# Kernel tuning notes

Measured on AMD Instinct MI355X. Metric: run time of the kernel, lower is better.

The kernel has to match this reference:

```python
import jax, jax.numpy as jnp
import numpy as np
from jax import lax

B, H, W = 2, 384, 384
NF = 64
SECTIONS = [2, 3, 4, 5, 6, 7, 8]  # radial core widths -> kernel sizes 3,5,7,9,11,13,15


def _radial_matrix(w):
    """Static [K,K,w] matrix mapping w radial core channels -> full KxK kernel,
    K = 2*w-1, replicating the torch nested-loop radial interpolation + flipcat."""
    mid = w - 1
    M = np.zeros((w, w, w), dtype=np.float32)
    for i in range(w):
        for j in range(w):
            d = np.sqrt(float((i - mid) ** 2 + (j - mid) ** 2))
            if d > mid:
                continue
            low, high = np.floor(d), np.ceil(d)
            if low == high:
                M[i, j, int(low)] = 1.0
            else:
                M[i, j, int(low)] = high - d
                M[i, j, int(low) + 1] = d - low
    # flipcat along both spatial dims: index order [0..w-1, w-2..0]
    q = mid - np.abs(np.arange(2 * w - 1) - mid)
    return M[q][:, q]  # [K, K, w]


def _conv(x, w, b):
    y = lax.conv_general_dilated(x, w, (1, 1), 'SAME',
                                 dimension_numbers=('NCHW', 'OIHW', 'NCHW'))
    return y + b[None, :, None, None]


def _resblock(x, wa, ba, wb, bb):
    return x + _conv(jax.nn.relu(_conv(x, wa, ba)), wb, bb)


def setup_inputs() -> dict:
    key = jax.random.key(0)
    ks = jax.random.split(key, 12)

    def wgt(k, shape):
        fan_in = shape[1] * shape[2] * shape[3]
        return jax.random.normal(k, shape, jnp.float32) / np.sqrt(fan_in)

    inp = {
        'data_with_est': jax.random.normal(ks[0], (B, 2, H, W), jnp.float32),
        'data': jax.random.normal(ks[1], (B, 1, H, W), jnp.float32),
        'w_first': wgt(ks[2], (NF, 2, 3, 3)), 'b_first': jnp.zeros((NF,), jnp.float32),
        'w1a': wgt(ks[3], (NF, NF, 3, 3)), 'b1a': jnp.zeros((NF,), jnp.float32),
        'w1b': wgt(ks[4], (NF, NF, 3, 3)), 'b1b': jnp.zeros((NF,), jnp.float32),
        'w2a': wgt(ks[5], (NF, NF, 3, 3)), 'b2a': jnp.zeros((NF,), jnp.float32),
        'w2b': wgt(ks[6], (NF, NF, 3, 3)), 'b2b': jnp.zeros((NF,), jnp.float32),
        'w3a': wgt(ks[7], (NF, NF, 3, 3)), 'b3a': jnp.zeros((NF,), jnp.float32),
        'w3b': wgt(ks[8], (NF, NF, 3, 3)), 'b3b': jnp.zeros((NF,), jnp.float32),
        'w_out': wgt(ks[9], (35, NF, 3, 3)), 'b_out': jnp.zeros((35,), jnp.float32),
    }
    return inp


def reference(data_with_est, data, w_first, b_first, w1a, b1a, w1b, b1b,
              w2a, b2a, w2b, b2b, w3a, b3a, w3b, b3b, w_out, b_out):
    # KPN backbone
    x = _conv(data_with_est, w_first, b_first)
    x = _resblock(x, w1a, b1a, w1b, b1b)
    x = _resblock(x, w2a, b2a, w2b, b2b)
    x = _resblock(x, w3a, b3a, w3b, b3b)
    core = _conv(x, w_out, b_out)  # [B, 35, H, W]

    frames = data[:, 0]  # [B, H, W]  (N=1, color=1)
    pred_img = jnp.zeros((B, H, W), core.dtype)
    off = 0
    for wsec in SECTIONS:
        K = 2 * wsec - 1
        r = K // 2
        M = jnp.asarray(_radial_matrix(wsec))  # [K, K, wsec]
        c = jnp.abs(lax.slice_in_dim(core, off, off + wsec, axis=1))  # [B, wsec, H, W]
        off += wsec
        # position-varying KxK kernel per pixel, softmax over the K*K taps
        kern = jnp.einsum('ijc,bchw->bijhw', M, c).reshape(B, K * K, H, W)
        kern = jax.nn.softmax(kern, axis=1)
        pad = jnp.pad(frames, ((0, 0), (r, r), (r, r)))
        # shifted neighborhood stack in torch loop order (i over rows, j over cols)
        patches = jnp.stack([pad[:, i:i + H, j:j + W]
                             for i in range(K) for j in range(K)], axis=1)
        pred_img = pred_img + jnp.sum(kern * patches, axis=1)
    return pred_img[:, None]  # [B, 1, H, W]
```

## Files before the change

### kernel.cpp

```cpp
#include <hip/hip_runtime.h>

#define HH 384
#define WW 384
#define BB 2

typedef unsigned short ushort_t;
typedef short  s16x8 __attribute__((ext_vector_type(8)));
typedef float  f32x4 __attribute__((ext_vector_type(4)));
typedef int    i32x4 __attribute__((ext_vector_type(4)));
typedef int    i32x2 __attribute__((ext_vector_type(2)));

union V16 { i32x4 i4; s16x8 v; ushort_t h[8]; };
union V8  { i32x2 i2; ushort_t h[4]; };

__device__ __forceinline__ ushort_t f2b(float f) {
    unsigned u = __builtin_bit_cast(unsigned, f);
    u += 0x7fffu + ((u >> 16) & 1u);
    return (ushort_t)(u >> 16);
}
__device__ __forceinline__ float b2f(ushort_t h) {
    return __builtin_bit_cast(float, ((unsigned)h) << 16);
}

struct WSrc { const float* p[8]; };

__global__ __launch_bounds__(256)
void repack_k(WSrc ws, ushort_t* __restrict__ Wd)
{
    const int idx = blockIdx.x * 256 + threadIdx.x;
    float val = 0.f;
    if (idx < 221184) {
        const int j = idx / 36864, rem = idx - j * 36864;
        const int i = rem & 7, lane = (rem >> 3) & 63;
        const int f = rem >> 9;
        const int mt = f & 3, st = f >> 2;
        const int t = st % 9, s = st / 9;
        const int co = mt * 16 + (lane & 15);
        const int ci = s * 32 + (lane >> 4) * 8 + i;
        val = ws.p[j][((size_t)(co * 64 + ci)) * 9 + t];
    } else if (idx < 248832) {
        const int rem = idx - 221184;
        const int i = rem & 7, lane = (rem >> 3) & 63;
        const int f = rem >> 9;
        const int mt = f % 3, st = f / 3;
        const int t = st % 9, s = st / 9;
        const int co = mt * 16 + (lane & 15);
        const int ci = s * 32 + (lane >> 4) * 8 + i;
        val = (co < 35) ? ws.p[6][((size_t)(co * 64 + ci)) * 9 + t] : 0.f;
    } else {
        const int rem = idx - 248832;
        const int i = rem & 7, lane = (rem >> 3) & 63;
        const int mt = rem >> 9;
        const int co = mt * 16 + (lane & 15);
        const int k = (lane >> 4) * 8 + i;
        if (k < 18) {
            const int ch = (k >= 9) ? 1 : 0;
            const int t = k - ch * 9;
            val = ws.p[7][((size_t)(co * 2 + ch)) * 9 + t];
        }
    }
    if (idx < 250880) Wd[idx] = f2b(val);
}

template<bool RELU, bool RES>
__global__ __launch_bounds__(256, 2)
void conv_mfma(const ushort_t* __restrict__ in, const ushort_t* __restrict__ wp,
               const float* __restrict__ bias, const ushort_t* __restrict__ res,
               ushort_t* __restrict__ out)
{
    __shared__ __align__(16) char smem[41472 + 36864];
    i32x4* s4 = (i32x4*)smem;
    i32x4* sw = (i32x4*)(smem + 41472);

    const int tid = threadIdx.x;
    const int x0 = blockIdx.x * 16, y0 = blockIdx.y * 16, b = blockIdx.z;
    const int lane = tid & 63, w4 = (tid >> 6) * 4;
    const int n = lane & 15, q = lane >> 4;

    {
        i32x4 ta[11];
#pragma unroll
        for (int k = 0; k < 11; ++k) {
            const int idx = tid + k * 256;
            ta[k] = 0;
            if (idx < 2592) {
                const int oct = idx & 7, p = idx >> 3;
                const int r = p / 18, xx = p - r * 18;
                const int gy = y0 - 1 + r, gx = x0 - 1 + xx;
                if ((unsigned)gy < HH && (unsigned)gx < WW)
                    ta[k] = *(const i32x4*)(in +
                        ((size_t)((b * HH + gy) * WW + gx)) * 64 + oct * 8);
            }
        }
        i32x4 tw[9];
#pragma unroll
        for (int k = 0; k < 9; ++k)
            tw[k] = *(const i32x4*)(wp + (size_t)(tid + k * 256) * 8);
#pragma unroll
        for (int k = 0; k < 11; ++k) {
            const int idx = tid + k * 256;
            if (idx < 2592) {
                const int oct = idx & 7, p = idx >> 3;
                const int r = p / 18, xx = p - r * 18;
                s4[(r * 8 + oct) * 18 + xx] = ta[k];
            }
        }
#pragma unroll
        for (int k = 0; k < 9; ++k)
            sw[tid + k * 256] = tw[k];
    }
    __syncthreads();

    f32x4 acc[4][4];
#pragma unroll
    for (int i = 0; i < 4; ++i)
#pragma unroll
        for (int j = 0; j < 4; ++j) acc[i][j] = 0.f;

    i32x4 pw[9];
#pragma unroll
    for (int k = 0; k < 9; ++k)
        pw[k] = *(const i32x4*)(wp + (size_t)(2304 + tid + k * 256) * 8);

#pragma unroll
    for (int t = 0; t < 9; ++t) {
        const int ky = t / 3, kx = t - ky * 3;
        V16 bf[4];
#pragma unroll
        for (int nt = 0; nt < 4; ++nt)
            bf[nt].i4 = s4[((w4 + nt + ky) * 8 + q) * 18 + (n + kx)];
#pragma unroll
        for (int mt = 0; mt < 4; ++mt) {
            V16 af; af.i4 = sw[(t * 4 + mt) * 64 + lane];
#pragma unroll
            for (int nt = 0; nt < 4; ++nt)
                acc[nt][mt] = __builtin_amdgcn_mfma_f32_16x16x32_bf16(
                    af.v, bf[nt].v, acc[nt][mt], 0, 0, 0);
        }
    }

    __syncthreads();
#pragma unroll
    for (int k = 0; k < 9; ++k)
        sw[tid + k * 256] = pw[k];
    __syncthreads();

#pragma unroll
    for (int t = 0; t < 9; ++t) {
        const int ky = t / 3, kx = t - ky * 3;
        V16 bf[4];
#pragma unroll
        for (int nt = 0; nt < 4; ++nt)
            bf[nt].i4 = s4[((w4 + nt + ky) * 8 + 4 + q) * 18 + (n + kx)];
#pragma unroll
        for (int mt = 0; mt < 4; ++mt) {
            V16 af; af.i4 = sw[(t * 4 + mt) * 64 + lane];
#pragma unroll
            for (int nt = 0; nt < 4; ++nt)
                acc[nt][mt] = __builtin_amdgcn_mfma_f32_16x16x32_bf16(
                    af.v, bf[nt].v, acc[nt][mt], 0, 0, 0);
        }
    }

    __syncthreads();
#pragma unroll
    for (int nt = 0; nt < 4; ++nt) {
        const int row = w4 + nt;
#pragma unroll
        for (int mt = 0; mt < 4; ++mt) {
            const int co0 = mt * 16 + q * 4;
            const float4 bv = *(const float4*)(bias + co0);
            float vv[4] = {acc[nt][mt][0] + bv.x, acc[nt][mt][1] + bv.y,
                           acc[nt][mt][2] + bv.z, acc[nt][mt][3] + bv.w};
            V8 ov;
#pragma unroll
            for (int r = 0; r < 4; ++r)
                ov.h[r] = f2b(RELU ? fmaxf(vv[r], 0.f) : vv[r]);
            const int c = 2 * mt + (q >> 1);
            const int cpr = c ^ (n & 7);
            *(i32x2*)(smem + row * 2048 + n * 128 + cpr * 16 + (q & 1) * 8) = ov.i2;
        }
    }
    __syncthreads();
#pragma unroll
    for (int r0 = 0; r0 < 4; ++r0) {
        const int row = w4 + r0, y = y0 + row;
#pragma unroll
        for (int j = 0; j < 2; ++j) {
            const int px = (lane >> 3) + 8 * j;
            const int clin = lane & 7;
            const int cpr = clin ^ (px & 7);
            V16 v;
            v.i4 = *(const i32x4*)(smem + row * 2048 + px * 128 + cpr * 16);
            const size_t goff = ((size_t)((b * HH + y) * WW + x0 + px)) * 64
                                + clin * 8;
            if (RES) {
                V16 rv;
                rv.i4 = *(const i32x4*)(res + goff);
#pragma unroll
                for (int e = 0; e < 8; ++e)
                    v.h[e] = f2b(b2f(v.h[e]) + b2f(rv.h[e]));
            }
            *(i32x4*)(out + goff) = v.i4;
        }
    }
}

__global__ __launch_bounds__(256, 4)
void conv_first(const float* __restrict__ in, const ushort_t* __restrict__ wp,
                const float* __restrict__ bias, ushort_t* __restrict__ out)
{
    __shared__ float s_raw[2][18][20];
    __shared__ __align__(16) char epi[32768];
    const int tid = threadIdx.x;
    const int x0 = blockIdx.x * 16, y0 = blockIdx.y * 16, b = blockIdx.z;
    {
        float tmp[3];
#pragma unroll
        for (int k = 0; k < 3; ++k) {
            const int idx = tid + k * 256;
            tmp[k] = 0.f;
            if (idx < 648) {
                const int ch = idx / 324, rem = idx - ch * 324;
                const int r = rem / 18, x = rem - r * 18;
                const int gy = y0 - 1 + r, gx = x0 - 1 + x;
                if ((unsigned)gy < HH && (unsigned)gx < WW)
                    tmp[k] = in[((size_t)((b * 2 + ch) * HH + gy)) * WW + gx];
            }
        }
#pragma unroll
        for (int k = 0; k < 3; ++k) {
            const int idx = tid + k * 256;
            if (idx < 648) {
                const int ch = idx / 324, rem = idx - ch * 324;
                const int r = rem / 18, x = rem - r * 18;
                s_raw[ch][r][x] = tmp[k];
            }
        }
    }
    __syncthreads();

    const int lane = tid & 63, w4 = (tid >> 6) * 4;
    const int n = lane & 15, q = lane >> 4;

    V16 af[4];
#pragma unroll
    for (int mt = 0; mt < 4; ++mt)
        af[mt].i4 = *(const i32x4*)(wp + ((size_t)(mt * 64 + lane)) * 8);

    f32x4 acc[4][4];
#pragma unroll
    for (int i = 0; i < 4; ++i)
#pragma unroll
        for (int j = 0; j < 4; ++j) acc[i][j] = 0.f;

#pragma unroll
    for (int nt = 0; nt < 4; ++nt) {
        const int r = w4 + nt;
        V16 bf;
#pragma unroll
        for (int i = 0; i < 8; ++i) {
            const int k = q * 8 + i;
            float v = 0.f;
            if (k < 18) {
                const int ch = (k >= 9) ? 1 : 0;
                const int t = k - ch * 9;
                const int ky = t / 3, kx = t - ky * 3;
                v = s_raw[ch][r + ky][n + kx];
            }
            bf.h[i] = f2b(v);
        }
#pragma unroll
        for (int mt = 0; mt < 4; ++mt)
            acc[nt][mt] = __builtin_amdgcn_mfma_f32_16x16x32_bf16(
                af[mt].v, bf.v, acc[nt][mt], 0, 0, 0);
    }

#pragma unroll
    for (int nt = 0; nt < 4; ++nt) {
        const int row = w4 + nt;
#pragma unroll
        for (int mt = 0; mt < 4; ++mt) {
            const int co0 = mt * 16 + q * 4;
            const float4 bv = *(const float4*)(bias + co0);
            V8 ov;
            ov.h[0] = f2b(acc[nt][mt][0] + bv.x);
            ov.h[1] = f2b(acc[nt][mt][1] + bv.y);
            ov.h[2] = f2b(acc[nt][mt][2] + bv.z);
            ov.h[3] = f2b(acc[nt][mt][3] + bv.w);
            const int c = 2 * mt + (q >> 1);
            const int cpr = c ^ (n & 7);
            *(i32x2*)(epi + row * 2048 + n * 128 + cpr * 16 + (q & 1) * 8) = ov.i2;
        }
    }
    __syncthreads();
#pragma unroll
    for (int r0 = 0; r0 < 4; ++r0) {
        const int row = w4 + r0, y = y0 + row;
#pragma unroll
        for (int j = 0; j < 2; ++j) {
            const int px = (lane >> 3) + 8 * j;
            const int clin = lane & 7;
            const int cpr = clin ^ (px & 7);
            i32x4 v = *(const i32x4*)(epi + row * 2048 + px * 128 + cpr * 16);
            *(i32x4*)(out + ((size_t)((b * HH + y) * WW + x0 + px)) * 64
                          + clin * 8) = v;
        }
    }
}

constexpr int isq_(int v) { int r = 0; while ((r + 1) * (r + 1) <= v) ++r; return r; }
constexpr double csqrt_(int x) {
    double g = x ? (double)x : 0.0;
    if (x) for (int i = 0; i < 80; ++i) g = 0.5 * (g + (double)x / g);
    return g;
}
constexpr int ringmult_(int m, int k) {
    if (m == 0) return 1;
    if (k == 0 || k == m) return 4;
    return 8;
}
constexpr int OFFS_(int s) {
    return s == 0 ? 0 : s == 1 ? 2 : s == 2 ? 5 : s == 3 ? 9
         : s == 4 ? 14 : s == 5 ? 20 : 27;
}

template<int M, int K>
__device__ __forceinline__ float ringsum(const float* s_f, int base)
{
    if constexpr (M == 0) {
        return s_f[base];
    } else if constexpr (K == 0) {
        return s_f[base + M * 48] + s_f[base - M * 48]
             + s_f[base + M]      + s_f[base - M];
    } else if constexpr (K == M) {
        return s_f[base + M * 48 + M] + s_f[base + M * 48 - M]
             + s_f[base - M * 48 + M] + s_f[base - M * 48 - M];
    } else {
        return s_f[base + M * 48 + K] + s_f[base + M * 48 - K]
             + s_f[base - M * 48 + K] + s_f[base - M * 48 - K]
             + s_f[base + K * 48 + M] + s_f[base + K * 48 - M]
             + s_f[base - K * 48 + M] + s_f[base - K * 48 - M];
    }
}

template<int M, int K, int S>
struct SecAcc {
    static __device__ __forceinline__ void run(const float* cv, float Sv,
                                               float* num, float* den) {
        constexpr int R = S + 1;
        if constexpr (R >= M) {
            constexpr int d2 = M * M + K * K;
            constexpr int mult = ringmult_(M, K);
            constexpr int OFF = OFFS_(S);
            if constexpr (d2 <= R * R) {
                constexpr int lo = isq_(d2);
                float v;
                if constexpr (lo * lo == d2) {
                    v = cv[OFF + lo];
                } else {
                    constexpr float fr = (float)(csqrt_(d2) - (double)lo);
                    v = __builtin_fmaf(fr, cv[OFF + lo + 1] - cv[OFF + lo],
                                       cv[OFF + lo]);
                }
                const float e = __expf(v);
                num[S] = __builtin_fmaf(e, Sv, num[S]);
                den[S] = __builtin_fmaf((float)mult, e, den[S]);
            } else {
                num[S] += Sv;
                den[S] += (float)mult;
            }
        }
        if constexpr (S < 6) SecAcc<M, K, S + 1>::run(cv, Sv, num, den);
    }
};

template<int M, int K>
struct RingK {
    static __device__ __forceinline__ void run(const float* cv, const float* s_f,
                                               int base, float* num, float* den) {
        const float Sv = ringsum<M, K>(s_f, base);
        SecAcc<M, K, 0>::run(cv, Sv, num, den);
        if constexpr (K < M) RingK<M, K + 1>::run(cv, s_f, base, num, den);
    }
};

template<int M>
struct RingLoop {
    static __device__ __forceinline__ void run(const float* cv, const float* s_f,
                                               int base, float* num, float* den) {
        RingK<M, 0>::run(cv, s_f, base, num, den);
        if constexpr (M < 7) RingLoop<M + 1>::run(cv, s_f, base, num, den);
    }
};

__global__ __launch_bounds__(256, 2)
void conv_kpn(const ushort_t* __restrict__ in, const ushort_t* __restrict__ wp,
              const float* __restrict__ bias, const float* __restrict__ frames,
              float* __restrict__ out)
{
    __shared__ __align__(16) char smem[41472 + 5760 + 27648];
    i32x4* s4 = (i32x4*)smem;
    float* s_core = (float*)smem;
    float* s_f = (float*)(smem + 41472);
    i32x4* sw = (i32x4*)(smem + 41472 + 5760);

    const int tid = threadIdx.x;
    const int x0 = blockIdx.x * 16, y0 = blockIdx.y * 16, b = blockIdx.z;

    {
        i32x4 ta[11];
#pragma unroll
        for (int k = 0; k < 11; ++k) {
            const int idx = tid + k * 256;
            ta[k] = 0;
            if (idx < 2592) {
                const int oct = idx & 7, p = idx >> 3;
                const int r = p / 18, xx = p - r * 18;
                const int gy = y0 - 1 + r, gx = x0 - 1 + xx;
                if ((unsigned)gy < HH && (unsigned)gx < WW)
                    ta[k] = *(const i32x4*)(in +
                        ((size_t)((b * HH + gy) * WW + gx)) * 64 + oct * 8);
            }
        }
        float ff[4];
#pragma unroll
        for (int k = 0; k < 4; ++k) {
            const int idx = tid + k * 256;
            ff[k] = 0.f;
            if (idx < 900) {
                const int r = idx / 30, c = idx - r * 30;
                const int y = y0 - 7 + r, x = x0 - 7 + c;
                if ((unsigned)y < HH && (unsigned)x < WW)
                    ff[k] = frames[((size_t)b * HH + y) * WW + x];
            }
        }
        i32x4 tw[7];
#pragma unroll
        for (int k = 0; k < 7; ++k) {
            const int idx = tid + k * 256;
            tw[k] = 0;
            if (idx < 1728)
                tw[k] = *(const i32x4*)(wp + (size_t)idx * 8);
        }
#pragma unroll
        for (int k = 0; k < 11; ++k) {
            const int idx = tid + k * 256;
            if (idx < 2592) {
                const int oct = idx & 7, p = idx >> 3;
                const int r = p / 18, xx = p - r * 18;
                s4[(r * 8 + oct) * 18 + xx] = ta[k];
            }
        }
#pragma unroll
        for (int k = 0; k < 4; ++k) {
            const int idx = tid + k * 256;
            if (idx < 900) {
                const int r = idx / 30, c = idx - r * 30;
                s_f[r * 48 + c] = ff[k];
            }
        }
#pragma unroll
        for (int k = 0; k < 7; ++k) {
            const int idx = tid + k * 256;
            if (idx < 1728) sw[idx] = tw[k];
        }
    }
    __syncthreads();

    const int lane = tid & 63, w4 = (tid >> 6) * 4;
    const int n = lane & 15, q = lane >> 4;

    f32x4 acc[4][3];
#pragma unroll
    for (int i = 0; i < 4; ++i)
#pragma unroll
        for (int j = 0; j < 3; ++j) acc[i][j] = 0.f;

    i32x4 pw[7];
#pragma unroll
    for (int k = 0; k < 7; ++k) {
        const int idx = tid + k * 256;
        pw[k] = 0;
        if (idx < 1728)
            pw[k] = *(const i32x4*)(wp + (size_t)(1728 + idx) * 8);
    }

#pragma unroll
    for (int t = 0; t < 9; ++t) {
        const int ky = t / 3, kx = t - ky * 3;
        V16 bf[4];
#pragma unroll
        for (int nt = 0; nt < 4; ++nt)
            bf[nt].i4 = s4[((w4 + nt + ky) * 8 + q) * 18 + (n + kx)];
#pragma unroll
        for (int mt = 0; mt < 3; ++mt) {
            V16 af; af.i4 = sw[(t * 3 + mt) * 64 + lane];
#pragma unroll
            for (int nt = 0; nt < 4; ++nt)
                acc[nt][mt] = __builtin_amdgcn_mfma_f32_16x16x32_bf16(
                    af.v, bf[nt].v, acc[nt][mt], 0, 0, 0);
        }
    }

    __syncthreads();
#pragma unroll
    for (int k = 0; k < 7; ++k) {
        const int idx = tid + k * 256;
        if (idx < 1728) sw[idx] = pw[k];
    }
    __syncthreads();

#pragma unroll
    for (int t = 0; t < 9; ++t) {
        const int ky = t / 3, kx = t - ky * 3;
        V16 bf[4];
#pragma unroll
        for (int nt = 0; nt < 4; ++nt)
            bf[nt].i4 = s4[((w4 + nt + ky) * 8 + 4 + q) * 18 + (n + kx)];
#pragma unroll
        for (int mt = 0; mt < 3; ++mt) {
            V16 af; af.i4 = sw[(t * 3 + mt) * 64 + lane];
#pragma unroll
            for (int nt = 0; nt < 4; ++nt)
                acc[nt][mt] = __builtin_amdgcn_mfma_f32_16x16x32_bf16(
                    af.v, bf[nt].v, acc[nt][mt], 0, 0, 0);
        }
    }

    __syncthreads();
#pragma unroll
    for (int nt = 0; nt < 4; ++nt) {
        const int px = (w4 + nt) * 16 + n;
#pragma unroll
        for (int mt = 0; mt < 3; ++mt) {
#pragma unroll
            for (int r = 0; r < 4; ++r) {
                const int ch = mt * 16 + q * 4 + r;
                if (ch < 35)
                    s_core[px * 37 + ch] = fabsf(acc[nt][mt][r] + bias[ch]);
            }
        }
    }
    __syncthreads();

    const int ty = tid >> 4, tx = tid & 15;
    const int base = (ty + 7) * 48 + (tx + 7);
    const float* cv = s_core + tid * 37;

    float num[7], den[7];
#pragma unroll
    for (int s = 0; s < 7; ++s) { num[s] = 0.f; den[s] = 0.f; }
    RingLoop<0>::run(cv, s_f, base, num, den);
    float pred = 0.f;
#pragma unroll
    for (int s = 0; s < 7; ++s) pred += num[s] / den[s];

    out[((size_t)b * HH + y0 + ty) * WW + x0 + tx] = pred;
}

extern "C" void kernel_launch(void* const* d_in, const int* in_sizes, int n_in,
                              void* d_out, int out_size, void* d_ws, size_t ws_size,
                              hipStream_t stream)
{
    const float* est     = (const float*)d_in[0];
    const float* data    = (const float*)d_in[1];
    const float* w_first = (const float*)d_in[2];
    const float* b_first = (const float*)d_in[3];
    const float* w1a = (const float*)d_in[4];
    const float* b1a = (const float*)d_in[5];
    const float* w1b = (const float*)d_in[6];
    const float* b1b = (const float*)d_in[7];
    const float* w2a = (const float*)d_in[8];
    const float* b2a = (const float*)d_in[9];
    const float* w2b = (const float*)d_in[10];
    const float* b2b = (const float*)d_in[11];
    const float* w3a = (const float*)d_in[12];
    const float* b3a = (const float*)d_in[13];
    const float* w3b = (const float*)d_in[14];
    const float* b3b = (const float*)d_in[15];
    const float* w_out = (const float*)d_in[16];
    const float* b_out = (const float*)d_in[17];

    ushort_t* X  = (ushort_t*)d_ws;
    ushort_t* T  = X + (size_t)BB * HH * WW * 64;
    ushort_t* Wd = T + (size_t)BB * HH * WW * 64;

    WSrc wsrc;
    wsrc.p[0] = w1a; wsrc.p[1] = w1b; wsrc.p[2] = w2a; wsrc.p[3] = w2b;
    wsrc.p[4] = w3a; wsrc.p[5] = w3b; wsrc.p[6] = w_out; wsrc.p[7] = w_first;

    dim3 blk(256), g(WW / 16, HH / 16, BB);
    repack_k<<<980, 256, 0, stream>>>(wsrc, Wd);
    conv_first<<<g, blk, 0, stream>>>(est, Wd + 248832, b_first, X);
    conv_mfma<true,  false><<<g, blk, 0, stream>>>(X, Wd + 0,      b1a, nullptr, T);
    conv_mfma<false, true ><<<g, blk, 0, stream>>>(T, Wd + 36864,  b1b, X, X);
    conv_mfma<true,  false><<<g, blk, 0, stream>>>(X, Wd + 73728,  b2a, nullptr, T);
    conv_mfma<false, true ><<<g, blk, 0, stream>>>(T, Wd + 110592, b2b, X, X);
    conv_mfma<true,  false><<<g, blk, 0, stream>>>(X, Wd + 147456, b3a, nullptr, T);
    conv_mfma<false, true ><<<g, blk, 0, stream>>>(T, Wd + 184320, b3b, X, X);
    conv_kpn<<<g, blk, 0, stream>>>(X, Wd + 221184, b_out, data, (float*)d_out);
}
```

Measured before the change: 316.4 us.

## Split conv LDS staging into channel halves to raise occupancy

The 3x3 conv kernels now stage only 32 input channels and a quarter (or half, for the output conv) of the packed weights in LDS at a time. The weight repack layout is reordered so each phase reads a contiguous chunk. LDS per block roughly halves, and launch bounds rise from 2 to 4 blocks per CU for the backbone convs and 3 for the KPN conv, aiming for more resident waves. In exchange there are extra barriers and serialized global reloads between phases, and prefetching of the next weights no longer overlaps the MFMA work.

```diff
diff --git a/kernel.cpp b/kernel.cpp
--- a/kernel.cpp
+++ b/kernel.cpp
@@ -33,8 +33,10 @@
         const int j = idx / 36864, rem = idx - j * 36864;
         const int i = rem & 7, lane = (rem >> 3) & 63;
         const int f = rem >> 9;
-        const int mt = f & 3, st = f >> 2;
-        const int t = st % 9, s = st / 9;
+        const int mtl = f & 1, g = f >> 1;
+        const int t = g % 9, smtH = g / 9;
+        const int mtH = smtH & 1, s = smtH >> 1;
+        const int mt = mtH * 2 + mtl;
         const int co = mt * 16 + (lane & 15);
         const int ci = s * 32 + (lane >> 4) * 8 + i;
         val = ws.p[j][((size_t)(co * 64 + ci)) * 9 + t];
@@ -63,14 +65,14 @@
 }
 
 template<bool RELU, bool RES>
-__global__ __launch_bounds__(256, 2)
+__global__ __launch_bounds__(256, 4)
 void conv_mfma(const ushort_t* __restrict__ in, const ushort_t* __restrict__ wp,
                const float* __restrict__ bias, const ushort_t* __restrict__ res,
                ushort_t* __restrict__ out)
 {
-    __shared__ __align__(16) char smem[41472 + 36864];
+    __shared__ __align__(16) char smem[20736 + 18432];
     i32x4* s4 = (i32x4*)smem;
-    i32x4* sw = (i32x4*)(smem + 41472);
+    i32x4* sw = (i32x4*)(smem + 20736);
 
     const int tid = threadIdx.x;
     const int x0 = blockIdx.x * 16, y0 = blockIdx.y * 16, b = blockIdx.z;
@@ -78,13 +80,13 @@
     const int n = lane & 15, q = lane >> 4;
 
     {
-        i32x4 ta[11];
-#pragma unroll
-        for (int k = 0; k < 11; ++k) {
+        i32x4 ta[6];
+#pragma unroll
+        for (int k = 0; k < 6; ++k) {
             const int idx = tid + k * 256;
             ta[k] = 0;
-            if (idx < 2592) {
-                const int oct = idx & 7, p = idx >> 3;
+            if (idx < 1296) {
+                const int oct = idx & 3, p = idx >> 2;
                 const int r = p / 18, xx = p - r * 18;
                 const int gy = y0 - 1 + r, gx = x0 - 1 + xx;
                 if ((unsigned)gy < HH && (unsigned)gx < WW)
@@ -92,22 +94,27 @@
                         ((size_t)((b * HH + gy) * WW + gx)) * 64 + oct * 8);
             }
         }
-        i32x4 tw[9];
-#pragma unroll
-        for (int k = 0; k < 9; ++k)
-            tw[k] = *(const i32x4*)(wp + (size_t)(tid + k * 256) * 8);
-#pragma unroll
-        for (int k = 0; k < 11; ++k) {
-            const int idx = tid + k * 256;
-            if (idx < 2592) {
-                const int oct = idx & 7, p = idx >> 3;
+        i32x4 tw[5];
+#pragma unroll
+        for (int k = 0; k < 5; ++k) {
+            const int idx = tid + k * 256;
+            tw[k] = 0;
+            if (idx < 1152) tw[k] = *(const i32x4*)(wp + (size_t)idx * 8);
+        }
+#pragma unroll
+        for (int k = 0; k < 6; ++k) {
+            const int idx = tid + k * 256;
+            if (idx < 1296) {
+                const int oct = idx & 3, p = idx >> 2;
                 const int r = p / 18, xx = p - r * 18;
-                s4[(r * 8 + oct) * 18 + xx] = ta[k];
-            }
-        }
-#pragma unroll
-        for (int k = 0; k < 9; ++k)
-            sw[tid + k * 256] = tw[k];
+                s4[(r * 4 + oct) * 18 + xx] = ta[k];
+            }
+        }
+#pragma unroll
+        for (int k = 0; k < 5; ++k) {
+            const int idx = tid + k * 256;
+            if (idx < 1152) sw[idx] = tw[k];
+        }
     }
     __syncthreads();
 
@@ -117,48 +124,83 @@
 #pragma unroll
         for (int j = 0; j < 4; ++j) acc[i][j] = 0.f;
 
-    i32x4 pw[9];
-#pragma unroll
-    for (int k = 0; k < 9; ++k)
-        pw[k] = *(const i32x4*)(wp + (size_t)(2304 + tid + k * 256) * 8);
-
-#pragma unroll
-    for (int t = 0; t < 9; ++t) {
-        const int ky = t / 3, kx = t - ky * 3;
-        V16 bf[4];
-#pragma unroll
-        for (int nt = 0; nt < 4; ++nt)
-            bf[nt].i4 = s4[((w4 + nt + ky) * 8 + q) * 18 + (n + kx)];
-#pragma unroll
-        for (int mt = 0; mt < 4; ++mt) {
-            V16 af; af.i4 = sw[(t * 4 + mt) * 64 + lane];
+#pragma unroll
+    for (int ph = 0; ph < 4; ++ph) {
+        const int mtH = ph & 1;
+#pragma unroll
+        for (int t = 0; t < 9; ++t) {
+            const int ky = t / 3, kx = t - ky * 3;
+            V16 bf[4];
 #pragma unroll
             for (int nt = 0; nt < 4; ++nt)
-                acc[nt][mt] = __builtin_amdgcn_mfma_f32_16x16x32_bf16(
-                    af.v, bf[nt].v, acc[nt][mt], 0, 0, 0);
-        }
-    }
-
-    __syncthreads();
-#pragma unroll
-    for (int k = 0; k < 9; ++k)
-        sw[tid + k * 256] = pw[k];
-    __syncthreads();
-
-#pragma unroll
-    for (int t = 0; t < 9; ++t) {
-        const int ky = t / 3, kx = t - ky * 3;
-        V16 bf[4];
-#pragma unroll
-        for (int nt = 0; nt < 4; ++nt)
-            bf[nt].i4 = s4[((w4 + nt + ky) * 8 + 4 + q) * 18 + (n + kx)];
-#pragma unroll
-        for (int mt = 0; mt < 4; ++mt) {
-            V16 af; af.i4 = sw[(t * 4 + mt) * 64 + lane];
-#pragma unroll
-            for (int nt = 0; nt < 4; ++nt)
-                acc[nt][mt] = __builtin_amdgcn_mfma_f32_16x16x32_bf16(
-                    af.v, bf[nt].v, acc[nt][mt], 0, 0, 0);
+                bf[nt].i4 = s4[((w4 + nt + ky) * 4 + q) * 18 + (n + kx)];
+#pragma unroll
+            for (int mtl = 0; mtl < 2; ++mtl) {
+                V16 af; af.i4 = sw[(t * 2 + mtl) * 64 + lane];
+#pragma unroll
+                for (int nt = 0; nt < 4; ++nt)
+                    acc[nt][mtH * 2 + mtl] = __builtin_amdgcn_mfma_f32_16x16x32_bf16(
+                        af.v, bf[nt].v, acc[nt][mtH * 2 + mtl], 0, 0, 0);
+            }
+        }
+        if (ph < 3) {
+            __syncthreads();
+            if (ph == 1) {
+                i32x4 ta[6];
+#pragma unroll
+                for (int k = 0; k < 6; ++k) {
+                    const int idx = tid + k * 256;
+                    ta[k] = 0;
+                    if (idx < 1296) {
+                        const int oct = idx & 3, p = idx >> 2;
+                        const int r = p / 18, xx = p - r * 18;
+                        const int gy = y0 - 1 + r, gx = x0 - 1 + xx;
+                        if ((unsigned)gy < HH && (unsigned)gx < WW)
+                            ta[k] = *(const i32x4*)(in +
+                                ((size_t)((b * HH + gy) * WW + gx)) * 64
+                                + 32 + oct * 8);
+                    }
+                }
+                i32x4 tw[5];
+#pragma unroll
+                for (int k = 0; k < 5; ++k) {
+                    const int idx = tid + k * 256;
+                    tw[k] = 0;
+                    if (idx < 1152)
+                        tw[k] = *(const i32x4*)(wp +
+                            (size_t)(1152 * (ph + 1) + idx) * 8);
+                }
+#pragma unroll
+                for (int k = 0; k < 6; ++k) {
+                    const int idx = tid + k * 256;
+                    if (idx < 1296) {
+                        const int oct = idx & 3, p = idx >> 2;
+                        const int r = p / 18, xx = p - r * 18;
+                        s4[(r * 4 + oct) * 18 + xx] = ta[k];
+                    }
+                }
+#pragma unroll
+                for (int k = 0; k < 5; ++k) {
+                    const int idx = tid + k * 256;
+                    if (idx < 1152) sw[idx] = tw[k];
+                }
+            } else {
+                i32x4 tw[5];
+#pragma unroll
+                for (int k = 0; k < 5; ++k) {
+                    const int idx = tid + k * 256;
+                    tw[k] = 0;
+                    if (idx < 1152)
+                        tw[k] = *(const i32x4*)(wp +
+                            (size_t)(1152 * (ph + 1) + idx) * 8);
+                }
+#pragma unroll
+                for (int k = 0; k < 5; ++k) {
+                    const int idx = tid + k * 256;
+                    if (idx < 1152) sw[idx] = tw[k];
+                }
+            }
+            __syncthreads();
         }
     }
 
@@ -394,28 +436,28 @@
     }
 };
 
-__global__ __launch_bounds__(256, 2)
+__global__ __launch_bounds__(256, 3)
 void conv_kpn(const ushort_t* __restrict__ in, const ushort_t* __restrict__ wp,
               const float* __restrict__ bias, const float* __restrict__ frames,
               float* __restrict__ out)
 {
-    __shared__ __align__(16) char smem[41472 + 5760 + 27648];
+    __shared__ __align__(16) char smem[20736 + 27648 + 5760];
     i32x4* s4 = (i32x4*)smem;
+    i32x4* sw = (i32x4*)(smem + 20736);
+    float* s_f = (float*)(smem + 48384);
     float* s_core = (float*)smem;
-    float* s_f = (float*)(smem + 41472);
-    i32x4* sw = (i32x4*)(smem + 41472 + 5760);
 
     const int tid = threadIdx.x;
     const int x0 = blockIdx.x * 16, y0 = blockIdx.y * 16, b = blockIdx.z;
 
     {
-        i32x4 ta[11];
-#pragma unroll
-        for (int k = 0; k < 11; ++k) {
+        i32x4 ta[6];
+#pragma unroll
+        for (int k = 0; k < 6; ++k) {
             const int idx = tid + k * 256;
             ta[k] = 0;
-            if (idx < 2592) {
-                const int oct = idx & 7, p = idx >> 3;
+            if (idx < 1296) {
+                const int oct = idx & 3, p = idx >> 2;
                 const int r = p / 18, xx = p - r * 18;
                 const int gy = y0 - 1 + r, gx = x0 - 1 + xx;
                 if ((unsigned)gy < HH && (unsigned)gx < WW)
@@ -444,12 +486,12 @@
                 tw[k] = *(const i32x4*)(wp + (size_t)idx * 8);
         }
 #pragma unroll
-        for (int k = 0; k < 11; ++k) {
-            const int idx = tid + k * 256;
-            if (idx < 2592) {
-                const int oct = idx & 7, p = idx >> 3;
+        for (int k = 0; k < 6; ++k) {
+            const int idx = tid + k * 256;
+            if (idx < 1296) {
+                const int oct = idx & 3, p = idx >> 2;
                 const int r = p / 18, xx = p - r * 18;
-                s4[(r * 8 + oct) * 18 + xx] = ta[k];
+                s4[(r * 4 + oct) * 18 + xx] = ta[k];
             }
         }
 #pragma unroll
@@ -477,22 +519,13 @@
 #pragma unroll
         for (int j = 0; j < 3; ++j) acc[i][j] = 0.f;
 
-    i32x4 pw[7];
-#pragma unroll
-    for (int k = 0; k < 7; ++k) {
-        const int idx = tid + k * 256;
-        pw[k] = 0;
-        if (idx < 1728)
-            pw[k] = *(const i32x4*)(wp + (size_t)(1728 + idx) * 8);
-    }
-
 #pragma unroll
     for (int t = 0; t < 9; ++t) {
         const int ky = t / 3, kx = t - ky * 3;
         V16 bf[4];
 #pragma unroll
         for (int nt = 0; nt < 4; ++nt)
-            bf[nt].i4 = s4[((w4 + nt + ky) * 8 + q) * 18 + (n + kx)];
+            bf[nt].i4 = s4[((w4 + nt + ky) * 4 + q) * 18 + (n + kx)];
 #pragma unroll
         for (int mt = 0; mt < 3; ++mt) {
             V16 af; af.i4 = sw[(t * 3 + mt) * 64 + lane];
@@ -504,10 +537,43 @@
     }
 
     __syncthreads();
-#pragma unroll
-    for (int k = 0; k < 7; ++k) {
-        const int idx = tid + k * 256;
-        if (idx < 1728) sw[idx] = pw[k];
+    {
+        i32x4 ta[6];
+#pragma unroll
+        for (int k = 0; k < 6; ++k) {
+            const int idx = tid + k * 256;
+            ta[k] = 0;
+            if (idx < 1296) {
+                const int oct = idx & 3, p = idx >> 2;
+                const int r = p / 18, xx = p - r * 18;
+                const int gy = y0 - 1 + r, gx = x0 - 1 + xx;
+                if ((unsigned)gy < HH && (unsigned)gx < WW)
+                    ta[k] = *(const i32x4*)(in +
+                        ((size_t)((b * HH + gy) * WW + gx)) * 64 + 32 + oct * 8);
+            }
+        }
+        i32x4 tw[7];
+#pragma unroll
+        for (int k = 0; k < 7; ++k) {
+            const int idx = tid + k * 256;
+            tw[k] = 0;
+            if (idx < 1728)
+                tw[k] = *(const i32x4*)(wp + (size_t)(1728 + idx) * 8);
+        }
+#pragma unroll
+        for (int k = 0; k < 6; ++k) {
+            const int idx = tid + k * 256;
+            if (idx < 1296) {
+                const int oct = idx & 3, p = idx >> 2;
+                const int r = p / 18, xx = p - r * 18;
+                s4[(r * 4 + oct) * 18 + xx] = ta[k];
+            }
+        }
+#pragma unroll
+        for (int k = 0; k < 7; ++k) {
+            const int idx = tid + k * 256;
+            if (idx < 1728) sw[idx] = tw[k];
+        }
     }
     __syncthreads();
 
@@ -517,7 +583,7 @@
         V16 bf[4];
 #pragma unroll
         for (int nt = 0; nt < 4; ++nt)
-            bf[nt].i4 = s4[((w4 + nt + ky) * 8 + 4 + q) * 18 + (n + kx)];
+            bf[nt].i4 = s4[((w4 + nt + ky) * 4 + q) * 18 + (n + kx)];
 #pragma unroll
         for (int mt = 0; mt < 3; ++mt) {
             V16 af; af.i4 = sw[(t * 3 + mt) * 64 + lane];
```

Result: slower. 411.2 us (+30.0%).

## Load conv tiles directly into LDS and halve shared memory per block

Applied to the files above, without the earlier changes.

Replaces the register-staged global-to-LDS copies in the 3x3 conv kernels with direct global_load_lds transfers. The input tile is split into two 32-channel halves and the weights into quarter chunks that are reloaded between phases, and the weight repack order is changed to match. This cuts LDS per block so occupancy bounds can rise (2 to 4 for conv_mfma, 2 to 3 for conv_kpn) and drops the staging registers. In exchange it adds extra barriers and serialized reload phases with no overlap between loading and MFMA work.

```diff
diff --git a/kernel.cpp b/kernel.cpp
--- a/kernel.cpp
+++ b/kernel.cpp
@@ -20,6 +20,12 @@
 }
 __device__ __forceinline__ float b2f(ushort_t h) {
     return __builtin_bit_cast(float, ((unsigned)h) << 16);
+}
+
+__device__ __forceinline__ void gld16(const void* g, void* l) {
+    __builtin_amdgcn_global_load_lds(
+        (const __attribute__((address_space(1))) void*)g,
+        (__attribute__((address_space(3))) void*)l, 16, 0, 0);
 }
 
 struct WSrc { const float* p[8]; };
@@ -33,8 +39,10 @@
         const int j = idx / 36864, rem = idx - j * 36864;
         const int i = rem & 7, lane = (rem >> 3) & 63;
         const int f = rem >> 9;
-        const int mt = f & 3, st = f >> 2;
-        const int t = st % 9, s = st / 9;
+        const int mtl = f & 1, g = f >> 1;
+        const int t = g % 9, smtH = g / 9;
+        const int mtH = smtH & 1, s = smtH >> 1;
+        const int mt = mtH * 2 + mtl;
         const int co = mt * 16 + (lane & 15);
         const int ci = s * 32 + (lane >> 4) * 8 + i;
         val = ws.p[j][((size_t)(co * 64 + ci)) * 9 + t];
@@ -63,51 +71,41 @@
 }
 
 template<bool RELU, bool RES>
-__global__ __launch_bounds__(256, 2)
+__global__ __launch_bounds__(256, 4)
 void conv_mfma(const ushort_t* __restrict__ in, const ushort_t* __restrict__ wp,
                const float* __restrict__ bias, const ushort_t* __restrict__ res,
                ushort_t* __restrict__ out)
 {
-    __shared__ __align__(16) char smem[41472 + 36864];
+    __shared__ __align__(16) char smem[20736 + 18432];
     i32x4* s4 = (i32x4*)smem;
-    i32x4* sw = (i32x4*)(smem + 41472);
+    i32x4* sw = (i32x4*)(smem + 20736);
 
     const int tid = threadIdx.x;
     const int x0 = blockIdx.x * 16, y0 = blockIdx.y * 16, b = blockIdx.z;
     const int lane = tid & 63, w4 = (tid >> 6) * 4;
     const int n = lane & 15, q = lane >> 4;
-
-    {
-        i32x4 ta[11];
-#pragma unroll
-        for (int k = 0; k < 11; ++k) {
-            const int idx = tid + k * 256;
-            ta[k] = 0;
-            if (idx < 2592) {
-                const int oct = idx & 7, p = idx >> 3;
-                const int r = p / 18, xx = p - r * 18;
-                const int gy = y0 - 1 + r, gx = x0 - 1 + xx;
-                if ((unsigned)gy < HH && (unsigned)gx < WW)
-                    ta[k] = *(const i32x4*)(in +
-                        ((size_t)((b * HH + gy) * WW + gx)) * 64 + oct * 8);
-            }
-        }
-        i32x4 tw[9];
-#pragma unroll
-        for (int k = 0; k < 9; ++k)
-            tw[k] = *(const i32x4*)(wp + (size_t)(tid + k * 256) * 8);
-#pragma unroll
-        for (int k = 0; k < 11; ++k) {
-            const int idx = tid + k * 256;
-            if (idx < 2592) {
-                const int oct = idx & 7, p = idx >> 3;
-                const int r = p / 18, xx = p - r * 18;
-                s4[(r * 8 + oct) * 18 + xx] = ta[k];
-            }
-        }
-#pragma unroll
-        for (int k = 0; k < 9; ++k)
-            sw[tid + k * 256] = tw[k];
+    const int wb = tid & 192;
+
+#pragma unroll
+    for (int k = 0; k < 6; ++k) {
+        const int slot = tid + k * 256;
+        char* lb = smem + (size_t)(k * 256 + wb) * 16;
+        if (slot < 1296) {
+            const int ro = slot / 18, xx = slot - ro * 18;
+            const int r = ro >> 2, oct = ro & 3;
+            const int gy = y0 - 1 + r, gx = x0 - 1 + xx;
+            if ((unsigned)gy < HH && (unsigned)gx < WW)
+                gld16(in + ((size_t)((b * HH + gy) * WW + gx)) * 64 + oct * 8, lb);
+            else
+                s4[slot] = (i32x4)0;
+        }
+    }
+#pragma unroll
+    for (int k = 0; k < 5; ++k) {
+        const int slot = tid + k * 256;
+        char* lb = smem + 20736 + (size_t)(k * 256 + wb) * 16;
+        if (slot < 1152)
+            gld16(wp + (size_t)slot * 8, lb);
     }
     __syncthreads();
 
@@ -117,48 +115,50 @@
 #pragma unroll
         for (int j = 0; j < 4; ++j) acc[i][j] = 0.f;
 
-    i32x4 pw[9];
-#pragma unroll
-    for (int k = 0; k < 9; ++k)
-        pw[k] = *(const i32x4*)(wp + (size_t)(2304 + tid + k * 256) * 8);
-
-#pragma unroll
-    for (int t = 0; t < 9; ++t) {
-        const int ky = t / 3, kx = t - ky * 3;
-        V16 bf[4];
-#pragma unroll
-        for (int nt = 0; nt < 4; ++nt)
-            bf[nt].i4 = s4[((w4 + nt + ky) * 8 + q) * 18 + (n + kx)];
-#pragma unroll
-        for (int mt = 0; mt < 4; ++mt) {
-            V16 af; af.i4 = sw[(t * 4 + mt) * 64 + lane];
+#pragma unroll
+    for (int ph = 0; ph < 4; ++ph) {
+        const int mtH = ph & 1;
+#pragma unroll
+        for (int t = 0; t < 9; ++t) {
+            const int ky = t / 3, kx = t - ky * 3;
+            V16 bf[4];
 #pragma unroll
             for (int nt = 0; nt < 4; ++nt)
-                acc[nt][mt] = __builtin_amdgcn_mfma_f32_16x16x32_bf16(
-                    af.v, bf[nt].v, acc[nt][mt], 0, 0, 0);
-        }
-    }
-
-    __syncthreads();
-#pragma unroll
-    for (int k = 0; k < 9; ++k)
-        sw[tid + k * 256] = pw[k];
-    __syncthreads();
-
-#pragma unroll
-    for (int t = 0; t < 9; ++t) {
-        const int ky = t / 3, kx = t - ky * 3;
-        V16 bf[4];
-#pragma unroll
-        for (int nt = 0; nt < 4; ++nt)
-            bf[nt].i4 = s4[((w4 + nt + ky) * 8 + 4 + q) * 18 + (n + kx)];
-#pragma unroll
-        for (int mt = 0; mt < 4; ++mt) {
-            V16 af; af.i4 = sw[(t * 4 + mt) * 64 + lane];
-#pragma unroll
-            for (int nt = 0; nt < 4; ++nt)
-                acc[nt][mt] = __builtin_amdgcn_mfma_f32_16x16x32_bf16(
-                    af.v, bf[nt].v, acc[nt][mt], 0, 0, 0);
+                bf[nt].i4 = s4[((w4 + nt + ky) * 4 + q) * 18 + (n + kx)];
+#pragma unroll
+            for (int mtl = 0; mtl < 2; ++mtl) {
+                V16 af; af.i4 = sw[(t * 2 + mtl) * 64 + lane];
+#pragma unroll
+                for (int nt = 0; nt < 4; ++nt)
+                    acc[nt][mtH * 2 + mtl] = __builtin_amdgcn_mfma_f32_16x16x32_bf16(
+                        af.v, bf[nt].v, acc[nt][mtH * 2 + mtl], 0, 0, 0);
+            }
+        }
+        if (ph < 3) {
+            __syncthreads();
+            if (ph == 1) {
+#pragma unroll
+                for (int k = 0; k < 6; ++k) {
+                    const int slot = tid + k * 256;
+                    char* lb = smem + (size_t)(k * 256 + wb) * 16;
+                    if (slot < 1296) {
+                        const int ro = slot / 18, xx = slot - ro * 18;
+                        const int r = ro >> 2, oct = ro & 3;
+                        const int gy = y0 - 1 + r, gx = x0 - 1 + xx;
+                        if ((unsigned)gy < HH && (unsigned)gx < WW)
+                            gld16(in + ((size_t)((b * HH + gy) * WW + gx)) * 64
+                                     + 32 + oct * 8, lb);
+                    }
+                }
+            }
+#pragma unroll
+            for (int k = 0; k < 5; ++k) {
+                const int slot = tid + k * 256;
+                char* lb = smem + 20736 + (size_t)(k * 256 + wb) * 16;
+                if (slot < 1152)
+                    gld16(wp + (size_t)(1152 * (ph + 1) + slot) * 8, lb);
+            }
+            __syncthreads();
         }
     }
 
@@ -394,35 +394,43 @@
     }
 };
 
-__global__ __launch_bounds__(256, 2)
+__global__ __launch_bounds__(256, 3)
 void conv_kpn(const ushort_t* __restrict__ in, const ushort_t* __restrict__ wp,
               const float* __restrict__ bias, const float* __restrict__ frames,
               float* __restrict__ out)
 {
-    __shared__ __align__(16) char smem[41472 + 5760 + 27648];
+    __shared__ __align__(16) char smem[20736 + 27648 + 5760];
     i32x4* s4 = (i32x4*)smem;
+    i32x4* sw = (i32x4*)(smem + 20736);
+    float* s_f = (float*)(smem + 48384);
     float* s_core = (float*)smem;
-    float* s_f = (float*)(smem + 41472);
-    i32x4* sw = (i32x4*)(smem + 41472 + 5760);
 
     const int tid = threadIdx.x;
     const int x0 = blockIdx.x * 16, y0 = blockIdx.y * 16, b = blockIdx.z;
-
+    const int wb = tid & 192;
+
+#pragma unroll
+    for (int k = 0; k < 6; ++k) {
+        const int slot = tid + k * 256;
+        char* lb = smem + (size_t)(k * 256 + wb) * 16;
+        if (slot < 1296) {
+            const int ro = slot / 18, xx = slot - ro * 18;
+            const int r = ro >> 2, oct = ro & 3;
+            const int gy = y0 - 1 + r, gx = x0 - 1 + xx;
+            if ((unsigned)gy < HH && (unsigned)gx < WW)
+                gld16(in + ((size_t)((b * HH + gy) * WW + gx)) * 64 + oct * 8, lb);
+            else
+                s4[slot] = (i32x4)0;
+        }
+    }
+#pragma unroll
+    for (int k = 0; k < 7; ++k) {
+        const int slot = tid + k * 256;
+        char* lb = smem + 20736 + (size_t)(k * 256 + wb) * 16;
+        if (slot < 1728)
+            gld16(wp + (size_t)slot * 8, lb);
+    }
     {
-        i32x4 ta[11];
-#pragma unroll
-        for (int k = 0; k < 11; ++k) {
-            const int idx = tid + k * 256;
-            ta[k] = 0;
-            if (idx < 2592) {
-                const int oct = idx & 7, p = idx >> 3;
-                const int r = p / 18, xx = p - r * 18;
-                const int gy = y0 - 1 + r, gx = x0 - 1 + xx;
-                if ((unsigned)gy < HH && (unsigned)gx < WW)
-                    ta[k] = *(const i32x4*)(in +
-                        ((size_t)((b * HH + gy) * WW + gx)) * 64 + oct * 8);
-            }
-        }
         float ff[4];
 #pragma unroll
         for (int k = 0; k < 4; ++k) {
@@ -435,23 +443,6 @@
                     ff[k] = frames[((size_t)b * HH + y) * WW + x];
             }
         }
-        i32x4 tw[7];
-#pragma unroll
-        for (int k = 0; k < 7; ++k) {
-            const int idx = tid + k * 256;
-            tw[k] = 0;
-            if (idx < 1728)
-                tw[k] = *(const i32x4*)(wp + (size_t)idx * 8);
-        }
-#pragma unroll
-        for (int k = 0; k < 11; ++k) {
-            const int idx = tid + k * 256;
-            if (idx < 2592) {
-                const int oct = idx & 7, p = idx >> 3;
-                const int r = p / 18, xx = p - r * 18;
-                s4[(r * 8 + oct) * 18 + xx] = ta[k];
-            }
-        }
 #pragma unroll
         for (int k = 0; k < 4; ++k) {
             const int idx = tid + k * 256;
@@ -460,11 +451,6 @@
                 s_f[r * 48 + c] = ff[k];
             }
         }
-#pragma unroll
-        for (int k = 0; k < 7; ++k) {
-            const int idx = tid + k * 256;
-            if (idx < 1728) sw[idx] = tw[k];
-        }
     }
     __syncthreads();
 
@@ -476,15 +462,6 @@
     for (int i = 0; i < 4; ++i)
 #pragma unroll
         for (int j = 0; j < 3; ++j) acc[i][j] = 0.f;
-
-    i32x4 pw[7];
-#pragma unroll
-    for (int k = 0; k < 7; ++k) {
-        const int idx = tid + k * 256;
-        pw[k] = 0;
-        if (idx < 1728)
-            pw[k] = *(const i32x4*)(wp + (size_t)(1728 + idx) * 8);
-    }
 
 #pragma unroll
     for (int t = 0; t < 9; ++t) {
@@ -492,7 +469,7 @@
         V16 bf[4];
 #pragma unroll
         for (int nt = 0; nt < 4; ++nt)
-            bf[nt].i4 = s4[((w4 + nt + ky) * 8 + q) * 18 + (n + kx)];
+            bf[nt].i4 = s4[((w4 + nt + ky) * 4 + q) * 18 + (n + kx)];
 #pragma unroll
         for (int mt = 0; mt < 3; ++mt) {
             V16 af; af.i4 = sw[(t * 3 + mt) * 64 + lane];
@@ -505,9 +482,24 @@
 
     __syncthreads();
 #pragma unroll
+    for (int k = 0; k < 6; ++k) {
+        const int slot = tid + k * 256;
+        char* lb = smem + (size_t)(k * 256 + wb) * 16;
+        if (slot < 1296) {
+            const int ro = slot / 18, xx = slot - ro * 18;
+            const int r = ro >> 2, oct = ro & 3;
+            const int gy = y0 - 1 + r, gx = x0 - 1 + xx;
+            if ((unsigned)gy < HH && (unsigned)gx < WW)
+                gld16(in + ((size_t)((b * HH + gy) * WW + gx)) * 64
+                         + 32 + oct * 8, lb);
+        }
+    }
+#pragma unroll
     for (int k = 0; k < 7; ++k) {
-        const int idx = tid + k * 256;
-        if (idx < 1728) sw[idx] = pw[k];
+        const int slot = tid + k * 256;
+        char* lb = smem + 20736 + (size_t)(k * 256 + wb) * 16;
+        if (slot < 1728)
+            gld16(wp + (size_t)(1728 + slot) * 8, lb);
     }
     __syncthreads();
 
@@ -517,7 +509,7 @@
         V16 bf[4];
 #pragma unroll
         for (int nt = 0; nt < 4; ++nt)
-            bf[nt].i4 = s4[((w4 + nt + ky) * 8 + 4 + q) * 18 + (n + kx)];
+            bf[nt].i4 = s4[((w4 + nt + ky) * 4 + q) * 18 + (n + kx)];
 #pragma unroll
         for (int mt = 0; mt < 3; ++mt) {
             V16 af; af.i4 = sw[(t * 3 + mt) * 64 + lane];
```

After: 336.1 us. 6.2% more time.
